# Kernel tuning notes

Measured on AMD Instinct MI355X. Metric: run time of the kernel, lower is better.

Reference implementation:

```python
import jax, jax.numpy as jnp
import numpy as np
from jax import lax

SHAPES = [(8, 64, 256, 256), (8, 128, 128, 128), (8, 256, 64, 64), (8, 512, 32, 32), (8, 512, 16, 16)]


def setup_inputs() -> dict:
    key = jax.random.key(0)
    keys = jax.random.split(key, 7)
    inp = {}
    for i, shp in enumerate(SHAPES):
        inp[f"t{i+1}"] = jax.random.normal(keys[i], shp, dtype=jnp.float32)
    inp["conv_w"] = jax.random.normal(keys[5], (1, 2, 7, 7), dtype=jnp.float32) * 0.1
    inp["conv_b"] = jax.random.normal(keys[6], (1,), dtype=jnp.float32) * 0.1
    return inp


def _spatial_att(t, w, b):
    # channel-wise mean+max -> [N,2,H,W]
    avg = jnp.mean(t, axis=1, keepdims=True)
    mx = jnp.max(t, axis=1, keepdims=True)
    x = jnp.concatenate([avg, mx], axis=1)
    # dilated 7x7 conv, dilation 3, pad 9 -> same HW
    y = lax.conv_general_dilated(
        x, w,
        window_strides=(1, 1),
        padding=((9, 9), (9, 9)),
        rhs_dilation=(3, 3),
        dimension_numbers=("NCHW", "OIHW", "NCHW"),
    ) + b.reshape(1, -1, 1, 1)
    return jax.nn.sigmoid(y)  # [N,1,H,W]


def reference(t1, t2, t3, t4, t5, conv_w, conv_b):
    outs = []
    for t in (t1, t2, t3, t4, t5):
        att = _spatial_att(t, conv_w, conv_b)
        outs.append(att * t + t)  # gate + residual
    return tuple(outs)
```

## Files before the change

kernel.cpp:

```cpp
#include <hip/hip_runtime.h>
#include <math.h>

#define DEVINL __device__ __forceinline__

DEVINL float4 ld4(const float* p) { return *reinterpret_cast<const float4*>(p); }
DEVINL void st4(float* p, const float4 v) { *reinterpret_cast<float4*>(p) = v; }
DEVINL float sigm(float v) { return 1.0f / (1.0f + expf(-v)); }

constexpr size_t O1 = 0;
constexpr size_t O2 = O1 + (size_t)8 * 64 * 256 * 256;
constexpr size_t O3 = O2 + (size_t)8 * 128 * 128 * 128;
constexpr size_t O4 = O3 + (size_t)8 * 256 * 64 * 64;
constexpr size_t O5 = O4 + (size_t)8 * 512 * 32 * 32;

constexpr size_t MAP1 = 0;
constexpr size_t MAP2 = MAP1 + (size_t)2 * 8 * 256 * 256;
constexpr size_t MAP3 = MAP2 + (size_t)2 * 8 * 128 * 128;
constexpr size_t MAP4 = MAP3 + (size_t)2 * 8 * 64 * 64;
constexpr size_t MAP5 = MAP4 + (size_t)2 * 8 * 32 * 32;
constexpr size_t ATT1 = MAP5 + (size_t)2 * 8 * 16 * 16;
constexpr size_t ATT2 = ATT1 + (size_t)8 * 256 * 256;
constexpr size_t ATT3 = ATT2 + (size_t)8 * 128 * 128;
constexpr size_t ATT4 = ATT3 + (size_t)8 * 64 * 64;
constexpr size_t ATT5 = ATT4 + (size_t)8 * 32 * 32;

template <int C, int HW>
DEVINL void reduce_simple(const float* __restrict__ in, float* __restrict__ map,
                          unsigned quad) {
  constexpr unsigned QPI = HW / 4;
  unsigned n = quad / QPI;
  unsigned hw0 = (quad & (QPI - 1)) * 4;
  const float* p = in + (size_t)n * ((size_t)C * HW) + hw0;
  float sx = 0.f, sy = 0.f, sz = 0.f, sw = 0.f;
  float mx = -3.402823466e38f, my = mx, mz = mx, mw = mx;
#pragma unroll 8
  for (int c = 0; c < C; ++c) {
    float4 v = ld4(p + (size_t)c * HW);
    sx += v.x; sy += v.y; sz += v.z; sw += v.w;
    mx = fmaxf(mx, v.x); my = fmaxf(my, v.y);
    mz = fmaxf(mz, v.z); mw = fmaxf(mw, v.w);
  }
  constexpr float inv = 1.0f / C;
  float* mp = map + (size_t)(n * (unsigned)HW + hw0) * 2;
  st4(mp,     make_float4(sx * inv, mx, sy * inv, my));
  st4(mp + 4, make_float4(sz * inv, mz, sw * inv, mw));
}

template <int C, int HW>
DEVINL void reduce_coop(const float* __restrict__ in, float* __restrict__ map,
                        float* s_red, unsigned blockLocal, unsigned tid) {
  constexpr unsigned QPI = HW / 4;
  constexpr int KCH = 8;
  constexpr int CPK = C / KCH;
  unsigned lane = tid & 31;
  unsigned k = tid >> 5;
  unsigned q = blockLocal * 32 + lane;
  unsigned n = q / QPI;
  unsigned hw0 = (q & (QPI - 1)) * 4;
  const float* p =
      in + (size_t)n * ((size_t)C * HW) + (size_t)(k * CPK) * HW + hw0;
  float sx = 0.f, sy = 0.f, sz = 0.f, sw = 0.f;
  float mx = -3.402823466e38f, my = mx, mz = mx, mw = mx;
#pragma unroll 8
  for (int c = 0; c < CPK; ++c) {
    float4 v = ld4(p + (size_t)c * HW);
    sx += v.x; sy += v.y; sz += v.z; sw += v.w;
    mx = fmaxf(mx, v.x); my = fmaxf(my, v.y);
    mz = fmaxf(mz, v.z); mw = fmaxf(mw, v.w);
  }
  float* slot = s_red + (k * 32 + lane) * 8;
  slot[0] = sx; slot[1] = sy; slot[2] = sz; slot[3] = sw;
  slot[4] = mx; slot[5] = my; slot[6] = mz; slot[7] = mw;
  __syncthreads();
  if (tid < 32) {
    float Sx = 0.f, Sy = 0.f, Sz = 0.f, Sw = 0.f;
    float Mx = -3.402823466e38f, My = Mx, Mz = Mx, Mw = Mx;
#pragma unroll
    for (int j = 0; j < KCH; ++j) {
      const float* sl = s_red + (j * 32 + tid) * 8;
      Sx += sl[0]; Sy += sl[1]; Sz += sl[2]; Sw += sl[3];
      Mx = fmaxf(Mx, sl[4]); My = fmaxf(My, sl[5]);
      Mz = fmaxf(Mz, sl[6]); Mw = fmaxf(Mw, sl[7]);
    }
    unsigned q2 = blockLocal * 32 + tid;
    unsigned n2 = q2 / QPI;
    unsigned hw2 = (q2 & (QPI - 1)) * 4;
    constexpr float inv = 1.0f / C;
    float* mp = map + (size_t)(n2 * (unsigned)HW + hw2) * 2;
    st4(mp,     make_float4(Sx * inv, Mx, Sy * inv, My));
    st4(mp + 4, make_float4(Sz * inv, Mz, Sw * inv, Mw));
  }
}

__global__ __launch_bounds__(256) void k_reduce(
    const float* __restrict__ t1, const float* __restrict__ t2,
    const float* __restrict__ t3, const float* __restrict__ t4,
    const float* __restrict__ t5, float* __restrict__ ws) {
  __shared__ float s_red[8 * 32 * 8];
  unsigned bid = blockIdx.x, tid = threadIdx.x;
  if (bid < 512) {
    reduce_simple<64, 65536>(t1, ws + MAP1, bid * 256 + tid);
  } else if (bid < 640) {
    reduce_simple<128, 16384>(t2, ws + MAP2, (bid - 512) * 256 + tid);
  } else if (bid < 672) {
    reduce_simple<256, 4096>(t3, ws + MAP3, (bid - 640) * 256 + tid);
  } else if (bid < 736) {
    reduce_coop<512, 1024>(t4, ws + MAP4, s_red, bid - 672, tid);
  } else {
    reduce_coop<512, 256>(t5, ws + MAP5, s_red, bid - 736, tid);
  }
}

template <int H, int W>
DEVINL void conv_one(const float* __restrict__ map, float* __restrict__ att,
                     const float* w_s, float bias, unsigned quad) {
  constexpr unsigned QPI = (H * W) / 4;
  unsigned n = quad / QPI;
  unsigned hw0 = (quad & (QPI - 1)) * 4;
  int h = (int)(hw0 / (unsigned)W);
  int w0 = (int)(hw0 & (unsigned)(W - 1));
  const float* base = map + (size_t)n * (2 * H * W);
  float acc[4] = {bias, bias, bias, bias};
#pragma unroll
  for (int ky = 0; ky < 7; ++ky) {
    int y = h + (ky - 3) * 3;
    if ((unsigned)y < (unsigned)H) {
      const float* row = base + (size_t)y * (2 * W);
      float rx[22], ry[22];
#pragma unroll
      for (int j = 0; j < 22; ++j) {
        int x = w0 - 9 + j;
        float2 v = make_float2(0.f, 0.f);
        if ((unsigned)x < (unsigned)W)
          v = *reinterpret_cast<const float2*>(row + 2 * x);
        rx[j] = v.x; ry[j] = v.y;
      }
#pragma unroll
      for (int kx = 0; kx < 7; ++kx) {
        float wa = w_s[ky * 7 + kx];
        float wm = w_s[49 + ky * 7 + kx];
#pragma unroll
        for (int i = 0; i < 4; ++i) {
          acc[i] = fmaf(wa, rx[i + 3 * kx], fmaf(wm, ry[i + 3 * kx], acc[i]));
        }
      }
    }
  }
  st4(att + (size_t)n * (H * W) + hw0,
      make_float4(sigm(acc[0]), sigm(acc[1]), sigm(acc[2]), sigm(acc[3])));
}

__global__ __launch_bounds__(256) void k_conv(float* __restrict__ ws,
                                              const float* __restrict__ cw,
                                              const float* __restrict__ cb) {
  __shared__ float w_s[98];
  unsigned bid = blockIdx.x, tid = threadIdx.x;
  if (tid < 98) w_s[tid] = cw[tid];
  __syncthreads();
  float bias = cb[0];
  if (bid < 512) {
    conv_one<256, 256>(ws + MAP1, ws + ATT1, w_s, bias, bid * 256 + tid);
  } else if (bid < 640) {
    conv_one<128, 128>(ws + MAP2, ws + ATT2, w_s, bias, (bid - 512) * 256 + tid);
  } else if (bid < 672) {
    conv_one<64, 64>(ws + MAP3, ws + ATT3, w_s, bias, (bid - 640) * 256 + tid);
  } else if (bid < 680) {
    conv_one<32, 32>(ws + MAP4, ws + ATT4, w_s, bias, (bid - 672) * 256 + tid);
  } else {
    conv_one<16, 16>(ws + MAP5, ws + ATT5, w_s, bias, (bid - 680) * 256 + tid);
  }
}

template <int C, int HW>
DEVINL void apply_four(const float* __restrict__ in, const float* __restrict__ att,
                       float* __restrict__ out, unsigned blockLocal, unsigned tid) {
#pragma unroll
  for (int j = 0; j < 4; ++j) {
    unsigned quad = blockLocal * 1024 + j * 256 + tid;
    size_t e = (size_t)quad * 4;
    unsigned hw0 = (unsigned)(e & (size_t)(HW - 1));
    unsigned n = (unsigned)(e / ((size_t)C * HW));
    float4 a = ld4(att + (size_t)n * HW + hw0);
    float4 t = ld4(in + e);
    st4(out + e, make_float4(fmaf(t.x, a.x, t.x), fmaf(t.y, a.y, t.y),
                             fmaf(t.z, a.z, t.z), fmaf(t.w, a.w, t.w)));
  }
}

__global__ __launch_bounds__(256) void k_apply(
    const float* __restrict__ t1, const float* __restrict__ t2,
    const float* __restrict__ t3, const float* __restrict__ t4,
    const float* __restrict__ t5, const float* __restrict__ ws,
    float* __restrict__ out) {
  unsigned bid = blockIdx.x, tid = threadIdx.x;
  if (bid < 8192) {
    apply_four<64, 65536>(t1, ws + ATT1, out + O1, bid, tid);
  } else if (bid < 12288) {
    apply_four<128, 16384>(t2, ws + ATT2, out + O2, bid - 8192, tid);
  } else if (bid < 14336) {
    apply_four<256, 4096>(t3, ws + ATT3, out + O3, bid - 12288, tid);
  } else if (bid < 15360) {
    apply_four<512, 1024>(t4, ws + ATT4, out + O4, bid - 14336, tid);
  } else {
    apply_four<512, 256>(t5, ws + ATT5, out + O5, bid - 15360, tid);
  }
}

extern "C" void kernel_launch(void* const* d_in, const int* in_sizes, int n_in,
                              void* d_out, int out_size, void* d_ws, size_t ws_size,
                              hipStream_t stream) {
  const float* t1 = (const float*)d_in[0];
  const float* t2 = (const float*)d_in[1];
  const float* t3 = (const float*)d_in[2];
  const float* t4 = (const float*)d_in[3];
  const float* t5 = (const float*)d_in[4];
  const float* cw = (const float*)d_in[5];
  const float* cb = (const float*)d_in[6];
  float* out = (float*)d_out;
  float* ws = (float*)d_ws;

  k_reduce<<<752, 256, 0, stream>>>(t1, t2, t3, t4, t5, ws);
  k_conv<<<682, 256, 0, stream>>>(ws, cw, cb);
  k_apply<<<15616, 256, 0, stream>>>(t1, t2, t3, t4, t5, ws, out);
}
```

Measured before the change: 503.5 us.

## Split channel reduction across half-waves and use nontemporal streaming in apply

The reduce kernel for the first three tensors now splits the channel loop between the two 32-lane halves of each wavefront and combines partial sums and maxes with a cross-half shuffle. This doubles the reduce block count so more loads are in flight per pixel. The apply kernel processes eight float4s per thread instead of four and uses nontemporal loads and stores for the large input and output streams, which is meant to reduce cache pollution and cut per-block overhead. The trade-offs are fewer apply blocks and possible loss of L2 reuse of the inputs between the reduce and apply passes.

```diff
diff --git a/kernel.cpp b/kernel.cpp
--- a/kernel.cpp
+++ b/kernel.cpp
@@ -3,8 +3,16 @@
 
 #define DEVINL __device__ __forceinline__
 
+typedef float f4 __attribute__((ext_vector_type(4)));
+
 DEVINL float4 ld4(const float* p) { return *reinterpret_cast<const float4*>(p); }
 DEVINL void st4(float* p, const float4 v) { *reinterpret_cast<float4*>(p) = v; }
+DEVINL f4 ldnt4(const float* p) {
+  return __builtin_nontemporal_load(reinterpret_cast<const f4*>(p));
+}
+DEVINL void stnt4(float* p, f4 v) {
+  __builtin_nontemporal_store(v, reinterpret_cast<f4*>(p));
+}
 DEVINL float sigm(float v) { return 1.0f / (1.0f + expf(-v)); }
 
 constexpr size_t O1 = 0;
@@ -25,25 +33,37 @@
 constexpr size_t ATT5 = ATT4 + (size_t)8 * 32 * 32;
 
 template <int C, int HW>
-DEVINL void reduce_simple(const float* __restrict__ in, float* __restrict__ map,
-                          unsigned quad) {
+DEVINL void reduce_shfl(const float* __restrict__ in, float* __restrict__ map,
+                        unsigned blockLocal, unsigned tid) {
   constexpr unsigned QPI = HW / 4;
-  unsigned n = quad / QPI;
-  unsigned hw0 = (quad & (QPI - 1)) * 4;
-  const float* p = in + (size_t)n * ((size_t)C * HW) + hw0;
+  unsigned wave = tid >> 6;
+  unsigned lane = tid & 63;
+  unsigned half = lane >> 5;
+  unsigned qlane = lane & 31;
+  unsigned q = blockLocal * 128 + wave * 32 + qlane;
+  unsigned n = q / QPI;
+  unsigned hw0 = (q & (QPI - 1)) * 4;
+  const float* p = in + (size_t)n * ((size_t)C * HW) +
+                   (size_t)(half * (C / 2)) * HW + hw0;
   float sx = 0.f, sy = 0.f, sz = 0.f, sw = 0.f;
   float mx = -3.402823466e38f, my = mx, mz = mx, mw = mx;
 #pragma unroll 8
-  for (int c = 0; c < C; ++c) {
+  for (int c = 0; c < C / 2; ++c) {
     float4 v = ld4(p + (size_t)c * HW);
     sx += v.x; sy += v.y; sz += v.z; sw += v.w;
     mx = fmaxf(mx, v.x); my = fmaxf(my, v.y);
     mz = fmaxf(mz, v.z); mw = fmaxf(mw, v.w);
   }
+  sx += __shfl_xor(sx, 32); sy += __shfl_xor(sy, 32);
+  sz += __shfl_xor(sz, 32); sw += __shfl_xor(sw, 32);
+  mx = fmaxf(mx, __shfl_xor(mx, 32)); my = fmaxf(my, __shfl_xor(my, 32));
+  mz = fmaxf(mz, __shfl_xor(mz, 32)); mw = fmaxf(mw, __shfl_xor(mw, 32));
   constexpr float inv = 1.0f / C;
-  float* mp = map + (size_t)(n * (unsigned)HW + hw0) * 2;
-  st4(mp,     make_float4(sx * inv, mx, sy * inv, my));
-  st4(mp + 4, make_float4(sz * inv, mz, sw * inv, mw));
+  float* mp = map + (size_t)(n * (unsigned)HW + hw0) * 2 + half * 4;
+  if (half == 0)
+    st4(mp, make_float4(sx * inv, mx, sy * inv, my));
+  else
+    st4(mp, make_float4(sz * inv, mz, sw * inv, mw));
 }
 
 template <int C, int HW>
@@ -98,16 +118,16 @@
     const float* __restrict__ t5, float* __restrict__ ws) {
   __shared__ float s_red[8 * 32 * 8];
   unsigned bid = blockIdx.x, tid = threadIdx.x;
-  if (bid < 512) {
-    reduce_simple<64, 65536>(t1, ws + MAP1, bid * 256 + tid);
-  } else if (bid < 640) {
-    reduce_simple<128, 16384>(t2, ws + MAP2, (bid - 512) * 256 + tid);
-  } else if (bid < 672) {
-    reduce_simple<256, 4096>(t3, ws + MAP3, (bid - 640) * 256 + tid);
-  } else if (bid < 736) {
-    reduce_coop<512, 1024>(t4, ws + MAP4, s_red, bid - 672, tid);
+  if (bid < 1024) {
+    reduce_shfl<64, 65536>(t1, ws + MAP1, bid, tid);
+  } else if (bid < 1280) {
+    reduce_shfl<128, 16384>(t2, ws + MAP2, bid - 1024, tid);
+  } else if (bid < 1344) {
+    reduce_shfl<256, 4096>(t3, ws + MAP3, bid - 1280, tid);
+  } else if (bid < 1408) {
+    reduce_coop<512, 1024>(t4, ws + MAP4, s_red, bid - 1344, tid);
   } else {
-    reduce_coop<512, 256>(t5, ws + MAP5, s_red, bid - 736, tid);
+    reduce_coop<512, 256>(t5, ws + MAP5, s_red, bid - 1408, tid);
   }
 }
 
@@ -172,18 +192,22 @@
 }
 
 template <int C, int HW>
-DEVINL void apply_four(const float* __restrict__ in, const float* __restrict__ att,
-                       float* __restrict__ out, unsigned blockLocal, unsigned tid) {
-#pragma unroll
-  for (int j = 0; j < 4; ++j) {
-    unsigned quad = blockLocal * 1024 + j * 256 + tid;
+DEVINL void apply_eight(const float* __restrict__ in, const float* __restrict__ att,
+                        float* __restrict__ out, unsigned blockLocal, unsigned tid) {
+#pragma unroll
+  for (int j = 0; j < 8; ++j) {
+    unsigned quad = blockLocal * 2048 + j * 256 + tid;
     size_t e = (size_t)quad * 4;
     unsigned hw0 = (unsigned)(e & (size_t)(HW - 1));
     unsigned n = (unsigned)(e / ((size_t)C * HW));
-    float4 a = ld4(att + (size_t)n * HW + hw0);
-    float4 t = ld4(in + e);
-    st4(out + e, make_float4(fmaf(t.x, a.x, t.x), fmaf(t.y, a.y, t.y),
-                             fmaf(t.z, a.z, t.z), fmaf(t.w, a.w, t.w)));
+    f4 a = *reinterpret_cast<const f4*>(att + (size_t)n * HW + hw0);
+    f4 t = ldnt4(in + e);
+    f4 r;
+    r[0] = fmaf(t[0], a[0], t[0]);
+    r[1] = fmaf(t[1], a[1], t[1]);
+    r[2] = fmaf(t[2], a[2], t[2]);
+    r[3] = fmaf(t[3], a[3], t[3]);
+    stnt4(out + e, r);
   }
 }
 
@@ -193,16 +217,16 @@
     const float* __restrict__ t5, const float* __restrict__ ws,
     float* __restrict__ out) {
   unsigned bid = blockIdx.x, tid = threadIdx.x;
-  if (bid < 8192) {
-    apply_four<64, 65536>(t1, ws + ATT1, out + O1, bid, tid);
-  } else if (bid < 12288) {
-    apply_four<128, 16384>(t2, ws + ATT2, out + O2, bid - 8192, tid);
-  } else if (bid < 14336) {
-    apply_four<256, 4096>(t3, ws + ATT3, out + O3, bid - 12288, tid);
-  } else if (bid < 15360) {
-    apply_four<512, 1024>(t4, ws + ATT4, out + O4, bid - 14336, tid);
+  if (bid < 4096) {
+    apply_eight<64, 65536>(t1, ws + ATT1, out + O1, bid, tid);
+  } else if (bid < 6144) {
+    apply_eight<128, 16384>(t2, ws + ATT2, out + O2, bid - 4096, tid);
+  } else if (bid < 7168) {
+    apply_eight<256, 4096>(t3, ws + ATT3, out + O3, bid - 6144, tid);
+  } else if (bid < 7680) {
+    apply_eight<512, 1024>(t4, ws + ATT4, out + O4, bid - 7168, tid);
   } else {
-    apply_four<512, 256>(t5, ws + ATT5, out + O5, bid - 15360, tid);
+    apply_eight<512, 256>(t5, ws + ATT5, out + O5, bid - 7680, tid);
   }
 }
 
@@ -219,7 +243,7 @@
   float* out = (float*)d_out;
   float* ws = (float*)d_ws;
 
-  k_reduce<<<752, 256, 0, stream>>>(t1, t2, t3, t4, t5, ws);
+  k_reduce<<<1424, 256, 0, stream>>>(t1, t2, t3, t4, t5, ws);
   k_conv<<<682, 256, 0, stream>>>(ws, cw, cb);
-  k_apply<<<15616, 256, 0, stream>>>(t1, t2, t3, t4, t5, ws, out);
-}
+  k_apply<<<7808, 256, 0, stream>>>(t1, t2, t3, t4, t5, ws, out);
+}
```

Measured after the change: 485.6 us. -3.5%, faster.
